# Optimization experiments

Hardware: AMD Instinct MI355X
Metric: run time of the kernel (lower is better)

## Reference

```python
import math
import jax, jax.numpy as jnp
import numpy as np

NH = 16          # num attention heads
NOPE = 128       # qk_nope_head_dim
ROPE = 64        # qk_rope_head_dim
VD = 128         # v_head_dim
QLR = 1536       # q_lora_rank
IH = 8           # index_n_heads
ID = 128         # index_head_dim
TOPK = 8         # index_topk
EPS = 1e-5


def layernorm(x, w, b):
    mu = jnp.mean(x, axis=-1, keepdims=True)
    var = jnp.mean((x - mu) ** 2, axis=-1, keepdims=True)
    return (x - mu) * jax.lax.rsqrt(var + EPS) * w + b


def rope_tables(dim, end, base=10000.0):
    freqs = 1.0 / (base ** (jnp.arange(0, dim, 2, dtype=jnp.float32) / dim))  # [dim//2]
    t = jnp.arange(end, dtype=jnp.float32)
    f = jnp.outer(t, freqs)  # [end, dim//2]
    return jnp.cos(f), jnp.sin(f)


def apply_rope(x, cos, sin):
    # x: [b, h, s, d]; cos/sin: [s, d//2] (interleaved real/imag pairs)
    xr, xi = x[..., 0::2], x[..., 1::2]
    c = cos[None, None, :, :]
    s = sin[None, None, :, :]
    or_, oi = xr * c - xi * s, xr * s + xi * c
    return jnp.stack([or_, oi], axis=-1).reshape(x.shape)


def setup_inputs() -> dict:
    key = jax.random.key(0)
    ks = jax.random.split(key, 16)
    H = 2048
    B, S = 2, 2048
    w = lambda k, shp: (jax.random.normal(k, shp, dtype=jnp.float32) * 0.02)
    return {
        "x": jax.random.normal(ks[0], (B, S, H), dtype=jnp.float32),
        "W_cq": w(ks[1], (H, QLR)),
        "q_norm_w": jnp.ones((QLR,), jnp.float32),
        "q_norm_b": jnp.zeros((QLR,), jnp.float32),
        "W_q": w(ks[2], (QLR, NH * (NOPE + ROPE))),
        "W_ckv": w(ks[3], (H, NH * (NOPE + ROPE))),
        "kv_norm_w": jnp.ones((NOPE,), jnp.float32),
        "kv_norm_b": jnp.zeros((NOPE,), jnp.float32),
        "W_kv": w(ks[4], (NOPE, NOPE + VD)),
        "W_o": w(ks[5], (NH * VD, H)),
        "W_ip": w(ks[6], (H, IH * ID)),
        "W_ig": w(ks[7], (H, IH)),
        "W_sq": w(ks[8], (ID, ID)),
        "W_sk": w(ks[9], (ID, ID)),
        "W_sv": w(ks[10], (ID, ID)),
        "W_io": w(ks[11], (ID, H)),
    }


def _forward(x, W_cq, q_norm_w, q_norm_b, W_q, W_ckv, kv_norm_w, kv_norm_b,
             W_kv, W_o, W_ip, W_ig, W_sq, W_sk, W_sv, W_io):
    B, S, H = x.shape
    # --- MLA dense path ---
    qc = layernorm(x @ W_cq, q_norm_w, q_norm_b)                  # [B,S,QLR]
    qp = (qc @ W_q).reshape(B, S, NH, NOPE + ROPE).transpose(0, 2, 1, 3)
    q_nope, q_pe = qp[..., :NOPE], qp[..., NOPE:]
    kvc = (x @ W_ckv).reshape(B, S, NH, ROPE + NOPE).transpose(0, 2, 1, 3)
    k_pe, kv_nope = kvc[..., :ROPE], kvc[..., ROPE:]
    kv_n = layernorm(kv_nope, kv_norm_w, kv_norm_b)               # [B,NH,S,NOPE]
    kvp = kv_n @ W_kv                                             # [B,NH,S,NOPE+VD]
    k_nope, v = kvp[..., :NOPE], kvp[..., NOPE:]
    cos, sin = rope_tables(ROPE, S)
    q_pe = apply_rope(q_pe, cos, sin)
    k_pe = apply_rope(k_pe, cos, sin)
    q = jnp.concatenate([q_nope, q_pe], axis=-1)                  # [B,NH,S,192]
    k = jnp.concatenate([k_nope, k_pe], axis=-1)
    scale = 1.0 / math.sqrt(NOPE + ROPE)
    scores = jnp.einsum("bhqd,bhkd->bhqk", q, k) * scale
    causal = jnp.triu(jnp.ones((S, S), dtype=bool), k=1)
    scores = jnp.where(causal[None, None], -jnp.inf, scores)
    probs = jax.nn.softmax(scores.astype(jnp.float32), axis=-1).astype(q.dtype)
    attn = jnp.einsum("bhqk,bhkd->bhqd", probs, v)                # [B,NH,S,VD]
    # --- NSA sparse path (lightning indexer) ---
    ist = (x @ W_ip).reshape(B, S, IH, ID).transpose(0, 2, 1, 3)  # [B,IH,S,ID]
    gate = (x @ W_ig).transpose(0, 2, 1)                          # [B,IH,S]
    _, top_idx = jax.lax.top_k(gate, TOPK)                        # [B,IH,TOPK]
    sel = jnp.take_along_axis(ist, top_idx[..., None], axis=2)    # [B,IH,TOPK,ID]
    sq, sk, sv = sel @ W_sq, sel @ W_sk, sel @ W_sv
    ss = jnp.einsum("bhqd,bhkd->bhqk", sq, sk) / math.sqrt(ID)    # [B,IH,TOPK,TOPK]
    sp = jax.nn.softmax(ss.astype(jnp.float32), axis=-1).astype(sq.dtype)
    so = jnp.einsum("bhqk,bhkd->bhqd", sp, sv)                    # [B,IH,TOPK,ID]
    sparse_out = so @ W_io                                        # [B,IH,TOPK,H]
    io = sparse_out.mean(axis=2)[:, :, None, :VD]                 # [B,IH,1,VD]
    io = jnp.broadcast_to(io, (B, IH, S, VD))
    io = jnp.repeat(io, NH // IH, axis=1)                         # [B,NH,S,VD]
    attn = attn + io
    out = attn.transpose(0, 2, 1, 3).reshape(B, S, NH * VD) @ W_o
    return out


def reference(x, W_cq, q_norm_w, q_norm_b, W_q, W_ckv, kv_norm_w, kv_norm_b,
              W_kv, W_o, W_ip, W_ig, W_sq, W_sk, W_sv, W_io):
    return _forward(x, W_cq, q_norm_w, q_norm_b, W_q, W_ckv, kv_norm_w,
                    kv_norm_b, W_kv, W_o, W_ip, W_ig, W_sq, W_sk, W_sv, W_io)
```

## Files before the change

### kernel.cpp

```cpp
#include <hip/hip_runtime.h>
#include <hip/hip_bf16.h>
#include <math.h>

#define NH    16
#define NOPE  128
#define ROPED 64
#define VD    128
#define QLR   1536
#define IH    8
#define ID    128
#define TOPK  8
#define EPSF  1e-5f
#define B_    2
#define S_    2048
#define H_    2048

using bf16 = __hip_bfloat16;
typedef __attribute__((ext_vector_type(8))) short short8;
typedef __attribute__((ext_vector_type(4))) short short4v;
typedef __attribute__((ext_vector_type(4))) float f32x4;

#define GLOBAL_AS __attribute__((address_space(1)))
#define LDS_AS    __attribute__((address_space(3)))

__device__ __forceinline__ float b2f(bf16 v) { return __bfloat162float(v); }
__device__ __forceinline__ bf16 f2b(float v) { return __float2bfloat16(v); }
__device__ __forceinline__ void stoC(float* p, float v) { *p = v; }
__device__ __forceinline__ void stoC(bf16* p, float v) { *p = __float2bfloat16(v); }

__global__ __launch_bounds__(256) void gate_k(const float* __restrict__ x,
                                              const float* __restrict__ Wg,
                                              float* __restrict__ gate) {
    const int t = threadIdx.x;
    const int wid = t >> 6, lane = t & 63;
    const int row = blockIdx.x * 4 + wid;
    const float* xp = x + (size_t)row * H_;

    float acc[8] = {};
    for (int k0 = 0; k0 < H_; k0 += 256) {
        const int kb = k0 + lane * 4;
        const f32x4 xv = *(const f32x4*)(xp + kb);
        const f32x4 w0 = *(const f32x4*)(Wg + (size_t)kb * 8);
        const f32x4 w1 = *(const f32x4*)(Wg + (size_t)kb * 8 + 4);
        const f32x4 w2 = *(const f32x4*)(Wg + (size_t)(kb + 1) * 8);
        const f32x4 w3 = *(const f32x4*)(Wg + (size_t)(kb + 1) * 8 + 4);
        const f32x4 w4 = *(const f32x4*)(Wg + (size_t)(kb + 2) * 8);
        const f32x4 w5 = *(const f32x4*)(Wg + (size_t)(kb + 2) * 8 + 4);
        const f32x4 w6 = *(const f32x4*)(Wg + (size_t)(kb + 3) * 8);
        const f32x4 w7 = *(const f32x4*)(Wg + (size_t)(kb + 3) * 8 + 4);
#pragma unroll
        for (int j = 0; j < 4; j++) {
            acc[j]     += xv[0] * w0[j] + xv[1] * w2[j] + xv[2] * w4[j] + xv[3] * w6[j];
            acc[4 + j] += xv[0] * w1[j] + xv[1] * w3[j] + xv[2] * w5[j] + xv[3] * w7[j];
        }
    }
#pragma unroll
    for (int j = 0; j < 8; j++) {
#pragma unroll
        for (int off = 32; off > 0; off >>= 1)
            acc[j] += __shfl_xor(acc[j], off);
    }
    if (lane == 0) {
#pragma unroll
        for (int j = 0; j < 8; j++) gate[(size_t)row * 8 + j] = acc[j];
    }
}

template <typename OT>
__global__ __launch_bounds__(256) void gemm_bt_mfma_k(const bf16* __restrict__ A,
                                                      const bf16* __restrict__ Bt,
                                                      OT* __restrict__ C,
                                                      int M, int N, int K) {
    __shared__ bf16 As[128 * 32];
    __shared__ bf16 Bs[128 * 32];
    const int t = threadIdx.x;
    const int w = t >> 6;
    const int l = t & 63;
    const int col = l & 15;
    const int quad = l >> 4;
    const int wm = w >> 1, wn = w & 1;

    const int gx = gridDim.x;
    const int nwg = gx * gridDim.y;
    const int lin = blockIdx.y * gx + blockIdx.x;
    const int work = (lin & 7) * (nwg >> 3) + (lin >> 3);
    const int row0 = (work / gx) * 128;
    const int col0 = (work % gx) * 128;

    const int rA = l >> 2;
    const int cA = (l & 3) * 8;
    const bf16* ga0 = A + (size_t)(row0 + w * 16 + rA) * K + cA;
    const bf16* ga1 = A + (size_t)(row0 + (4 + w) * 16 + rA) * K + cA;
    const bf16* gb0 = Bt + (size_t)(col0 + w * 16 + rA) * K + cA;
    const bf16* gb1 = Bt + (size_t)(col0 + (4 + w) * 16 + rA) * K + cA;
    bf16* lA0 = &As[w * 512];
    bf16* lA1 = &As[(4 + w) * 512];
    bf16* lB0 = &Bs[w * 512];
    bf16* lB1 = &Bs[(4 + w) * 512];

    f32x4 acc[4][4];
#pragma unroll
    for (int i = 0; i < 4; i++)
#pragma unroll
        for (int j = 0; j < 4; j++) acc[i][j] = (f32x4){0.f, 0.f, 0.f, 0.f};

    for (int k0 = 0; k0 < K; k0 += 32) {
        __syncthreads();
        __builtin_amdgcn_global_load_lds((const GLOBAL_AS void*)(ga0 + k0),
                                         (LDS_AS void*)lA0, 16, 0, 0);
        __builtin_amdgcn_global_load_lds((const GLOBAL_AS void*)(ga1 + k0),
                                         (LDS_AS void*)lA1, 16, 0, 0);
        __builtin_amdgcn_global_load_lds((const GLOBAL_AS void*)(gb0 + k0),
                                         (LDS_AS void*)lB0, 16, 0, 0);
        __builtin_amdgcn_global_load_lds((const GLOBAL_AS void*)(gb1 + k0),
                                         (LDS_AS void*)lB1, 16, 0, 0);
        __syncthreads();

        short8 af[4], bfr[4];
#pragma unroll
        for (int i = 0; i < 4; i++) {
            af[i]  = *(const short8*)&As[(wm * 64 + i * 16 + col) * 32 + quad * 8];
            bfr[i] = *(const short8*)&Bs[(wn * 64 + i * 16 + col) * 32 + quad * 8];
        }
#pragma unroll
        for (int i = 0; i < 4; i++)
#pragma unroll
            for (int j = 0; j < 4; j++)
                acc[i][j] = __builtin_amdgcn_mfma_f32_16x16x32_bf16(af[i], bfr[j], acc[i][j], 0, 0, 0);
    }

#pragma unroll
    for (int i = 0; i < 4; i++)
#pragma unroll
        for (int j = 0; j < 4; j++)
#pragma unroll
            for (int r = 0; r < 4; r++) {
                const int gr = row0 + wm * 64 + i * 16 + quad * 4 + r;
                const int gc = col0 + wn * 64 + j * 16 + col;
                stoC(C + (size_t)gr * N + gc, acc[i][j][r]);
            }
}

__global__ __launch_bounds__(256) void gemm_kv_k(const bf16* __restrict__ A,
                                                 const bf16* __restrict__ Bt,
                                                 bf16* __restrict__ kvc,
                                                 bf16* __restrict__ VbT) {
    __shared__ bf16 As[128 * 32];
    __shared__ bf16 Bs[128 * 32];
    const int K = 128;
    const int t = threadIdx.x;
    const int w = t >> 6;
    const int l = t & 63;
    const int col = l & 15;
    const int quad = l >> 4;
    const int wm = w >> 1, wn = w & 1;

    const int gx = gridDim.x;
    const int nwg = gx * gridDim.y;
    const int lin = blockIdx.y * gx + blockIdx.x;
    const int work = (lin & 7) * (nwg >> 3) + (lin >> 3);
    const int row0 = (work / gx) * 128;
    const int col0 = (work % gx) * 128;

    const int rA = l >> 2;
    const int cA = (l & 3) * 8;
    const bf16* ga0 = A + (size_t)(row0 + w * 16 + rA) * K + cA;
    const bf16* ga1 = A + (size_t)(row0 + (4 + w) * 16 + rA) * K + cA;
    const bf16* gb0 = Bt + (size_t)(col0 + w * 16 + rA) * K + cA;
    const bf16* gb1 = Bt + (size_t)(col0 + (4 + w) * 16 + rA) * K + cA;
    bf16* lA0 = &As[w * 512];
    bf16* lA1 = &As[(4 + w) * 512];
    bf16* lB0 = &Bs[w * 512];
    bf16* lB1 = &Bs[(4 + w) * 512];

    f32x4 acc[4][4];
#pragma unroll
    for (int i = 0; i < 4; i++)
#pragma unroll
        for (int j = 0; j < 4; j++) acc[i][j] = (f32x4){0.f, 0.f, 0.f, 0.f};

    for (int k0 = 0; k0 < K; k0 += 32) {
        __syncthreads();
        __builtin_amdgcn_global_load_lds((const GLOBAL_AS void*)(ga0 + k0),
                                         (LDS_AS void*)lA0, 16, 0, 0);
        __builtin_amdgcn_global_load_lds((const GLOBAL_AS void*)(ga1 + k0),
                                         (LDS_AS void*)lA1, 16, 0, 0);
        __builtin_amdgcn_global_load_lds((const GLOBAL_AS void*)(gb0 + k0),
                                         (LDS_AS void*)lB0, 16, 0, 0);
        __builtin_amdgcn_global_load_lds((const GLOBAL_AS void*)(gb1 + k0),
                                         (LDS_AS void*)lB1, 16, 0, 0);
        __syncthreads();

        short8 af[4], bfr[4];
#pragma unroll
        for (int i = 0; i < 4; i++) {
            af[i]  = *(const short8*)&As[(wm * 64 + i * 16 + col) * 32 + quad * 8];
            bfr[i] = *(const short8*)&Bs[(wn * 64 + i * 16 + col) * 32 + quad * 8];
        }
#pragma unroll
        for (int i = 0; i < 4; i++)
#pragma unroll
            for (int j = 0; j < 4; j++)
                acc[i][j] = __builtin_amdgcn_mfma_f32_16x16x32_bf16(af[i], bfr[j], acc[i][j], 0, 0, 0);
    }

    if (col0 == 0) {
#pragma unroll
        for (int i = 0; i < 4; i++)
#pragma unroll
            for (int j = 0; j < 4; j++)
#pragma unroll
                for (int r = 0; r < 4; r++) {
                    const int gr = row0 + wm * 64 + i * 16 + quad * 4 + r;
                    const int gc = wn * 64 + j * 16 + col;
                    kvc[(size_t)gr * 192 + gc] = f2b(acc[i][j][r]);
                }
    } else {
        const int bb = row0 >> 15;
        const int ssb = ((row0 >> 4) & (S_ - 1)) + wm * 4;
#pragma unroll
        for (int j = 0; j < 4; j++) {
            const int dv = wn * 64 + j * 16 + col;
#pragma unroll
            for (int r = 0; r < 4; r++) {
                const int hh = quad * 4 + r;
                short4v pk;
#pragma unroll
                for (int i = 0; i < 4; i++) {
                    bf16 v = f2b(acc[i][j][r]);
                    pk[i] = *(short*)&v;
                }
                *(short4v*)&VbT[((size_t)(bb * NH + hh) * 128 + dv) * S_ + ssb] = pk;
            }
        }
    }
}

__global__ __launch_bounds__(256) void kv_ln_k(bf16* __restrict__ kvc,
                                               const float* __restrict__ knw,
                                               const float* __restrict__ knb,
                                               bf16* __restrict__ kvn) {
    const int idx = blockIdx.x * 4 + (threadIdx.x >> 6);
    const int lane = threadIdx.x & 63;
    const int s = (idx >> 4) & (S_ - 1);
    const size_t base = (size_t)idx * 192;

    const float v0 = b2f(kvc[base + 64 + lane]);
    const float v1 = b2f(kvc[base + 128 + lane]);
    float xr = 0.f, xi = 0.f;
    if (lane < 32) { xr = b2f(kvc[base + 2 * lane]); xi = b2f(kvc[base + 2 * lane + 1]); }

    float s1 = v0 + v1, s2 = v0 * v0 + v1 * v1;
#pragma unroll
    for (int off = 32; off > 0; off >>= 1) {
        s1 += __shfl_xor(s1, off);
        s2 += __shfl_xor(s2, off);
    }
    const float mu = s1 * (1.f / 128.f);
    const float rinv = rsqrtf(s2 * (1.f / 128.f) - mu * mu + EPSF);
    kvn[(size_t)idx * 128 + lane]      = f2b((v0 - mu) * rinv * knw[lane] + knb[lane]);
    kvn[(size_t)idx * 128 + lane + 64] = f2b((v1 - mu) * rinv * knw[lane + 64] + knb[lane + 64]);

    if (lane < 32) {
        const float freq = exp2f(-0.41524101186092014f * (float)lane);
        const float ang = (float)s * freq;
        float sn, c; sincosf(ang, &sn, &c);
        kvc[base + 128 + 2 * lane]     = f2b(xr * c - xi * sn);
        kvc[base + 128 + 2 * lane + 1] = f2b(xr * sn + xi * c);
    }
}

__global__ __launch_bounds__(256) void cast_bf16_k(const float* __restrict__ X,
                                                   bf16* __restrict__ Y, int n4) {
    for (int i = blockIdx.x * 256 + threadIdx.x; i < n4; i += gridDim.x * 256) {
        const f32x4 v = ((const f32x4*)X)[i];
        short4v o;
#pragma unroll
        for (int j = 0; j < 4; j++) {
            bf16 b = f2b(v[j]);
            o[j] = *(short*)&b;
        }
        ((short4v*)Y)[i] = o;
    }
}

__global__ __launch_bounds__(256) void transpose_cast_k(const float* __restrict__ W,
                                                        bf16* __restrict__ Wt,
                                                        int K, int N) {
    __shared__ float tile[32][33];
    const int t = threadIdx.x;
    const int tx = t & 31, ty = t >> 5;
    const int n0 = blockIdx.x * 32;
    const int k0 = blockIdx.y * 32;
#pragma unroll
    for (int i = 0; i < 4; i++)
        tile[ty + 8 * i][tx] = W[(size_t)(k0 + ty + 8 * i) * N + n0 + tx];
    __syncthreads();
#pragma unroll
    for (int i = 0; i < 4; i++)
        Wt[(size_t)(n0 + ty + 8 * i) * K + k0 + tx] = f2b(tile[tx][ty + 8 * i]);
}

__global__ __launch_bounds__(256) void layernorm_cast_k(const float* __restrict__ X,
                                                        const float* __restrict__ w,
                                                        const float* __restrict__ b,
                                                        bf16* __restrict__ Y,
                                                        int L) {
    __shared__ float r1[256], r2[256];
    const int row = blockIdx.x;
    const int t = threadIdx.x;
    const float* xp = X + (size_t)row * L;
    bf16* yp = Y + (size_t)row * L;
    float s1 = 0.f, s2 = 0.f;
    for (int j = t; j < L; j += 256) { const float v = xp[j]; s1 += v; s2 += v * v; }
    r1[t] = s1; r2[t] = s2; __syncthreads();
    for (int off = 128; off > 0; off >>= 1) {
        if (t < off) { r1[t] += r1[t + off]; r2[t] += r2[t + off]; }
        __syncthreads();
    }
    const float mu   = r1[0] / (float)L;
    const float var  = r2[0] / (float)L - mu * mu;
    const float rinv = rsqrtf(var + EPSF);
    for (int j = t; j < L; j += 256)
        yp[j] = f2b((xp[j] - mu) * rinv * w[j] + b[j]);
}

__global__ __launch_bounds__(256) void q_rope_k(bf16* __restrict__ qp) {
    const int total = B_ * S_ * NH * 32;
    for (int p = blockIdx.x * 256 + threadIdx.x; p < total; p += gridDim.x * 256) {
        const int j = p & 31;
        const int row = p >> 5;
        const int sr = row >> 4;
        const int s = sr & (S_ - 1);
        const size_t base = (size_t)row * 192 + 128 + 2 * j;
        const float xr = b2f(qp[base]);
        const float xi = b2f(qp[base + 1]);
        const float freq = exp2f(-0.41524101186092014f * (float)j);
        const float ang = (float)s * freq;
        float sn, c; sincosf(ang, &sn, &c);
        qp[base]     = f2b(xr * c - xi * sn);
        qp[base + 1] = f2b(xr * sn + xi * c);
    }
}

__global__ __launch_bounds__(256) void sparse_k(const float* __restrict__ gate,
                                                const float* __restrict__ ist,
                                                const float* __restrict__ Wsq,
                                                const float* __restrict__ Wsk,
                                                const float* __restrict__ Wsv,
                                                const float* __restrict__ Wio,
                                                float* __restrict__ io) {
    __shared__ float g[S_];
    __shared__ float sel[TOPK][ID];
    __shared__ float sq[TOPK][ID], sk[TOPK][ID], sv[TOPK][ID];
    __shared__ float sp[TOPK][TOPK];
    __shared__ float ms[ID];
    __shared__ float rv[256];
    __shared__ int ri[256];
    __shared__ int sidx[TOPK];
    const int bi = blockIdx.x;
    const int ih = bi % IH;
    const int b = bi / IH;
    const int t = threadIdx.x;

    for (int s = t; s < S_; s += 256) g[s] = gate[(size_t)(b * S_ + s) * IH + ih];
    __syncthreads();

    for (int r = 0; r < TOPK; r++) {
        float bv = -INFINITY; int bx = S_;
        for (int s = t; s < S_; s += 256) {
            const float v = g[s];
            if (v > bv) { bv = v; bx = s; }
        }
        rv[t] = bv; ri[t] = bx; __syncthreads();
        for (int off = 128; off > 0; off >>= 1) {
            if (t < off) {
                const float v2 = rv[t + off]; const int i2 = ri[t + off];
                if (v2 > rv[t] || (v2 == rv[t] && i2 < ri[t])) { rv[t] = v2; ri[t] = i2; }
            }
            __syncthreads();
        }
        if (t == 0) { sidx[r] = ri[0]; g[ri[0]] = -INFINITY; }
        __syncthreads();
    }

    for (int i = t; i < TOPK * ID; i += 256) {
        const int r = i >> 7, d = i & 127;
        sel[r][d] = ist[((size_t)(b * S_ + sidx[r]) * IH + ih) * ID + d];
    }
    __syncthreads();

    for (int i = t; i < TOPK * ID; i += 256) {
        const int r = i >> 7, n = i & 127;
        float aq = 0.f, ak = 0.f, av = 0.f;
        for (int k = 0; k < 128; k++) {
            const float s = sel[r][k];
            aq += s * Wsq[k * ID + n];
            ak += s * Wsk[k * ID + n];
            av += s * Wsv[k * ID + n];
        }
        sq[r][n] = aq; sk[r][n] = ak; sv[r][n] = av;
    }
    __syncthreads();

    if (t < TOPK * TOPK) {
        const int r = t >> 3, c = t & 7;
        float a = 0.f;
        for (int k = 0; k < 128; k++) a += sq[r][k] * sk[c][k];
        sp[r][c] = a * 0.08838834764831845f;
    }
    __syncthreads();

    if (t < TOPK) {
        float m = -INFINITY;
        for (int c = 0; c < 8; c++) m = fmaxf(m, sp[t][c]);
        float e[8]; float sum = 0.f;
        for (int c = 0; c < 8; c++) { e[c] = expf(sp[t][c] - m); sum += e[c]; }
        for (int c = 0; c < 8; c++) sp[t][c] = e[c] / sum;
    }
    __syncthreads();

    if (t < ID) {
        float acc = 0.f;
        for (int r = 0; r < 8; r++) {
            float so = 0.f;
            for (int c = 0; c < 8; c++) so += sp[r][c] * sv[c][t];
            acc += so;
        }
        ms[t] = acc * 0.125f;
    }
    __syncthreads();

    if (t < ID) {
        float acc = 0.f;
        for (int k = 0; k < 128; k++) acc += ms[k] * Wio[(size_t)k * H_ + t];
        io[((size_t)b * IH + ih) * ID + t] = acc;
    }
}

__global__ __launch_bounds__(256) void attn_mfma_k(const bf16* __restrict__ Qp,
                                                   const bf16* __restrict__ Kc,
                                                   const bf16* __restrict__ VbT,
                                                   const float* __restrict__ io,
                                                   bf16* __restrict__ O) {
    __shared__ unsigned short Kt[64 * 200];
    __shared__ unsigned short Vt[128 * 72];
    __shared__ unsigned short Ps[4 * 16 * 72];
    __shared__ float io_s[128];

    const int lin = blockIdx.x + 16 * blockIdx.y + 256 * blockIdx.z;
    const int swz = (lin & 7) * 64 + (lin >> 3);
    const int pairi = swz & 15;
    const int h = (swz >> 4) & 15;
    const int b = swz >> 8;

    const int t = threadIdx.x;
    const int lane = t & 63;
    const int wq = t >> 6;
    const int col = lane & 15;
    const int quad = lane >> 4;

    if (t < 128) io_s[t] = io[((size_t)b * IH + (h >> 1)) * ID + t];

    const float scale = 0.07216878364870322f;
    const bf16* vplane = VbT + (size_t)(b * NH + h) * 128 * (size_t)S_;

#pragma unroll 1
    for (int ti = 0; ti < 2; ti++) {
        const int qt = (ti == 0) ? pairi : 31 - pairi;
        const int q0 = qt * 64;

        short8 qfrag[6];
        {
            const int q = q0 + wq * 16 + col;
            const short8* qrow = (const short8*)(Qp + ((size_t)(b * S_ + q) * NH + h) * 192);
#pragma unroll
            for (int kc = 0; kc < 6; kc++) qfrag[kc] = qrow[kc * 4 + quad];
        }

        float m_r[4], l_r[4];
#pragma unroll
        for (int r = 0; r < 4; r++) { m_r[r] = -1e30f; l_r[r] = 0.f; }
        f32x4 accO[8];
#pragma unroll
        for (int nt = 0; nt < 8; nt++) accO[nt] = (f32x4){0.f, 0.f, 0.f, 0.f};

        const int nkt = qt + 1;

        for (int kt = 0; kt < nkt; kt++) {
            const int kt0 = kt * 64;
            __syncthreads();
            {
                const int kr = t >> 2;
                const int c0 = (t & 3) * 48;
                const short8* src = (const short8*)(Kc + ((size_t)(b * S_ + kt0 + kr) * NH + h) * 192 + c0);
                short8* dst = (short8*)&Kt[kr * 200 + c0];
#pragma unroll
                for (int c = 0; c < 6; c++) dst[c] = src[c];
            }
            {
                const int ki0 = (t & 7) * 8;
#pragma unroll
                for (int p = 0; p < 4; p++) {
                    const int dv = p * 32 + (t >> 3);
                    const short8 vv = *(const short8*)(vplane + (size_t)dv * S_ + kt0 + ki0);
                    *(short8*)&Vt[dv * 72 + ki0] = vv;
                }
            }
            __syncthreads();

            f32x4 s[4];
            __builtin_amdgcn_s_setprio(1);
#pragma unroll
            for (int nt = 0; nt < 4; nt++) {
                f32x4 acc = (f32x4){0.f, 0.f, 0.f, 0.f};
#pragma unroll
                for (int kc = 0; kc < 6; kc++) {
                    const short8 kf = *(const short8*)&Kt[(nt * 16 + col) * 200 + kc * 32 + quad * 8];
                    acc = __builtin_amdgcn_mfma_f32_16x16x32_bf16(qfrag[kc], kf, acc, 0, 0, 0);
                }
                s[nt] = acc;
            }
            __builtin_amdgcn_s_setprio(0);
#pragma unroll
            for (int nt = 0; nt < 4; nt++)
#pragma unroll
                for (int r = 0; r < 4; r++) {
                    const int kg = kt0 + nt * 16 + col;
                    const int qg = q0 + wq * 16 + quad * 4 + r;
                    const float v = s[nt][r] * scale;
                    s[nt][r] = (kg > qg) ? -1e30f : v;
                }
            float alpha[4];
#pragma unroll
            for (int r = 0; r < 4; r++) {
                float mt = fmaxf(fmaxf(s[0][r], s[1][r]), fmaxf(s[2][r], s[3][r]));
                mt = fmaxf(mt, __shfl_xor(mt, 1));
                mt = fmaxf(mt, __shfl_xor(mt, 2));
                mt = fmaxf(mt, __shfl_xor(mt, 4));
                mt = fmaxf(mt, __shfl_xor(mt, 8));
                const float mn = fmaxf(m_r[r], mt);
                alpha[r] = __expf(m_r[r] - mn);
                m_r[r] = mn;
                float rs = 0.f;
#pragma unroll
                for (int nt = 0; nt < 4; nt++) {
                    const float p = __expf(s[nt][r] - mn);
                    s[nt][r] = p;
                    rs += p;
                }
                rs += __shfl_xor(rs, 1);
                rs += __shfl_xor(rs, 2);
                rs += __shfl_xor(rs, 4);
                rs += __shfl_xor(rs, 8);
                l_r[r] = l_r[r] * alpha[r] + rs;
            }
            {
                unsigned short* pw = &Ps[wq * 1152];
#pragma unroll
                for (int nt = 0; nt < 4; nt++)
#pragma unroll
                    for (int r = 0; r < 4; r++) {
                        bf16 hv = f2b(s[nt][r]);
                        pw[(quad * 4 + r) * 72 + nt * 16 + col] = *(unsigned short*)&hv;
                    }
            }
            short8 pf[2];
#pragma unroll
            for (int kk = 0; kk < 2; kk++)
                pf[kk] = *(const short8*)&Ps[wq * 1152 + col * 72 + kk * 32 + quad * 8];
#pragma unroll
            for (int nt = 0; nt < 8; nt++)
#pragma unroll
                for (int r = 0; r < 4; r++) accO[nt][r] *= alpha[r];
            __builtin_amdgcn_s_setprio(1);
#pragma unroll
            for (int nt = 0; nt < 8; nt++) {
#pragma unroll
                for (int kk = 0; kk < 2; kk++) {
                    const short8 vf = *(const short8*)&Vt[(nt * 16 + col) * 72 + kk * 32 + quad * 8];
                    accO[nt] = __builtin_amdgcn_mfma_f32_16x16x32_bf16(pf[kk], vf, accO[nt], 0, 0, 0);
                }
            }
            __builtin_amdgcn_s_setprio(0);
        }

        float rinv[4];
#pragma unroll
        for (int r = 0; r < 4; r++) rinv[r] = 1.f / l_r[r];
#pragma unroll
        for (int nt = 0; nt < 8; nt++) {
            const int dv = nt * 16 + col;
            const float iov = io_s[dv];
#pragma unroll
            for (int r = 0; r < 4; r++) {
                const int q = q0 + wq * 16 + quad * 4 + r;
                O[((size_t)(b * S_ + q) * NH + h) * VD + dv] = f2b(accO[nt][r] * rinv[r] + iov);
            }
        }
    }
}

extern "C" void kernel_launch(void* const* d_in, const int* in_sizes, int n_in,
                              void* d_out, int out_size, void* d_ws, size_t ws_size,
                              hipStream_t stream) {
    const float* x      = (const float*)d_in[0];
    const float* W_cq   = (const float*)d_in[1];
    const float* qn_w   = (const float*)d_in[2];
    const float* qn_b   = (const float*)d_in[3];
    const float* W_q    = (const float*)d_in[4];
    const float* W_ckv  = (const float*)d_in[5];
    const float* kvn_w  = (const float*)d_in[6];
    const float* kvn_b  = (const float*)d_in[7];
    const float* W_kv   = (const float*)d_in[8];
    const float* W_o    = (const float*)d_in[9];
    const float* W_ip   = (const float*)d_in[10];
    const float* W_ig   = (const float*)d_in[11];
    const float* W_sq   = (const float*)d_in[12];
    const float* W_sk   = (const float*)d_in[13];
    const float* W_sv   = (const float*)d_in[14];
    const float* W_io   = (const float*)d_in[15];
    float* out = (float*)d_out;

    const int M = B_ * S_;

    char* wsb = (char*)d_ws;
    float* rbig  = (float*)wsb;
    bf16*  kvn   = (bf16*)(wsb + 16777216);
    bf16*  qp    = (bf16*)(wsb + 33554432);
    bf16*  kvc   = (bf16*)(wsb + 58720256);
    bf16*  cqb   = (bf16*)(wsb + 58720256);
    bf16*  VbT   = (bf16*)(wsb + 83886080);
    bf16*  Wt    = (bf16*)(wsb + 83886080);
    float* gate  = (float*)(wsb + 100663296);
    bf16*  WkvT  = (bf16*)(wsb + 100663296);
    float* iob   = (float*)(wsb + 100794368);
    float* cq    = rbig;
    float* ist   = rbig;
    bf16*  attnb = (bf16*)rbig;
    bf16*  xb    = (bf16*)d_out;

    dim3 blk(256);

    cast_bf16_k<<<dim3(2048), blk, 0, stream>>>(x, xb, M * H_ / 4);

    transpose_cast_k<<<dim3(QLR / 32, H_ / 32), blk, 0, stream>>>(W_cq, Wt, H_, QLR);
    gemm_bt_mfma_k<float><<<dim3(QLR / 128, M / 128), blk, 0, stream>>>(xb, Wt, cq, M, QLR, H_);
    layernorm_cast_k<<<dim3(M), blk, 0, stream>>>(cq, qn_w, qn_b, cqb, QLR);

    transpose_cast_k<<<dim3(3072 / 32, QLR / 32), blk, 0, stream>>>(W_q, Wt, QLR, 3072);
    gemm_bt_mfma_k<bf16><<<dim3(3072 / 128, M / 128), blk, 0, stream>>>(cqb, Wt, qp, M, 3072, QLR);

    transpose_cast_k<<<dim3(3072 / 32, H_ / 32), blk, 0, stream>>>(W_ckv, Wt, H_, 3072);
    gemm_bt_mfma_k<bf16><<<dim3(3072 / 128, M / 128), blk, 0, stream>>>(xb, Wt, kvc, M, 3072, H_);

    transpose_cast_k<<<dim3(1024 / 32, H_ / 32), blk, 0, stream>>>(W_ip, Wt, H_, 1024);
    gemm_bt_mfma_k<float><<<dim3(1024 / 128, M / 128), blk, 0, stream>>>(xb, Wt, ist, M, IH * ID, H_);

    gate_k<<<dim3(M / 4), blk, 0, stream>>>(x, W_ig, gate);

    q_rope_k<<<dim3(2048), blk, 0, stream>>>(qp);

    kv_ln_k<<<dim3(B_ * S_ * NH / 4), blk, 0, stream>>>(kvc, kvn_w, kvn_b, kvn);

    sparse_k<<<dim3(B_ * IH), blk, 0, stream>>>(gate, ist, W_sq, W_sk, W_sv, W_io, iob);

    transpose_cast_k<<<dim3(256 / 32, 128 / 32), blk, 0, stream>>>(W_kv, WkvT, 128, 256);
    gemm_kv_k<<<dim3(2, (B_ * S_ * NH) / 128), blk, 0, stream>>>(kvn, WkvT, kvc, VbT);

    attn_mfma_k<<<dim3(16, NH, B_), blk, 0, stream>>>(qp, kvc, VbT, iob, attnb);

    transpose_cast_k<<<dim3(H_ / 32, H_ / 32), blk, 0, stream>>>(W_o, Wt, H_, H_);
    gemm_bt_mfma_k<float><<<dim3(H_ / 128, M / 128), blk, 0, stream>>>(attnb, Wt, out, M, H_, H_);
}
```

Baseline: 685.1 us.

## Register-prefetch next K/V tile and skip rescaling with lazy softmax max

The attention kernel now loads the next K and V tile into registers while the current tile's MFMAs run, so global-load latency overlaps compute instead of stalling before each tile. The running-max update is made lazy: the max and the accumulator rescale only change when the new tile max exceeds the old one by more than a threshold. The launch bounds also request 3 blocks per CU, and the io values are read straight from global memory. The extra prefetch registers compete with the occupancy hint, which may cause spills, and the lazy max lets exponentials grow up to e^8 before rescaling.

```diff
diff --git a/kernel.cpp b/kernel.cpp
--- a/kernel.cpp
+++ b/kernel.cpp
@@ -438,15 +438,14 @@
     }
 }
 
-__global__ __launch_bounds__(256) void attn_mfma_k(const bf16* __restrict__ Qp,
-                                                   const bf16* __restrict__ Kc,
-                                                   const bf16* __restrict__ VbT,
-                                                   const float* __restrict__ io,
-                                                   bf16* __restrict__ O) {
+__global__ __launch_bounds__(256, 3) void attn_mfma_k(const bf16* __restrict__ Qp,
+                                                      const bf16* __restrict__ Kc,
+                                                      const bf16* __restrict__ VbT,
+                                                      const float* __restrict__ io,
+                                                      bf16* __restrict__ O) {
     __shared__ unsigned short Kt[64 * 200];
     __shared__ unsigned short Vt[128 * 72];
     __shared__ unsigned short Ps[4 * 16 * 72];
-    __shared__ float io_s[128];
 
     const int lin = blockIdx.x + 16 * blockIdx.y + 256 * blockIdx.z;
     const int swz = (lin & 7) * 64 + (lin >> 3);
@@ -460,10 +459,13 @@
     const int col = lane & 15;
     const int quad = lane >> 4;
 
-    if (t < 128) io_s[t] = io[((size_t)b * IH + (h >> 1)) * ID + t];
-
     const float scale = 0.07216878364870322f;
     const bf16* vplane = VbT + (size_t)(b * NH + h) * 128 * (size_t)S_;
+
+    const int kr = t >> 2;
+    const int kc0 = (t & 3) * 48;
+    const int vki0 = (t & 7) * 8;
+    const int vdv = t >> 3;
 
 #pragma unroll 1
     for (int ti = 0; ti < 2; ti++) {
@@ -487,27 +489,38 @@
 
         const int nkt = qt + 1;
 
+        short8 kreg[6], vreg[4];
+        {
+            const short8* ksrc = (const short8*)(Kc + ((size_t)(b * S_ + kr) * NH + h) * 192 + kc0);
+#pragma unroll
+            for (int c = 0; c < 6; c++) kreg[c] = ksrc[c];
+#pragma unroll
+            for (int p = 0; p < 4; p++)
+                vreg[p] = *(const short8*)(vplane + (size_t)(p * 32 + vdv) * S_ + vki0);
+        }
+
         for (int kt = 0; kt < nkt; kt++) {
             const int kt0 = kt * 64;
             __syncthreads();
             {
-                const int kr = t >> 2;
-                const int c0 = (t & 3) * 48;
-                const short8* src = (const short8*)(Kc + ((size_t)(b * S_ + kt0 + kr) * NH + h) * 192 + c0);
-                short8* dst = (short8*)&Kt[kr * 200 + c0];
-#pragma unroll
-                for (int c = 0; c < 6; c++) dst[c] = src[c];
-            }
-            {
-                const int ki0 = (t & 7) * 8;
-#pragma unroll
-                for (int p = 0; p < 4; p++) {
-                    const int dv = p * 32 + (t >> 3);
-                    const short8 vv = *(const short8*)(vplane + (size_t)dv * S_ + kt0 + ki0);
-                    *(short8*)&Vt[dv * 72 + ki0] = vv;
-                }
+                short8* dst = (short8*)&Kt[kr * 200 + kc0];
+#pragma unroll
+                for (int c = 0; c < 6; c++) dst[c] = kreg[c];
+#pragma unroll
+                for (int p = 0; p < 4; p++)
+                    *(short8*)&Vt[(p * 32 + vdv) * 72 + vki0] = vreg[p];
             }
             __syncthreads();
+
+            if (kt + 1 < nkt) {
+                const int nk0 = kt0 + 64;
+                const short8* ksrc = (const short8*)(Kc + ((size_t)(b * S_ + nk0 + kr) * NH + h) * 192 + kc0);
+#pragma unroll
+                for (int c = 0; c < 6; c++) kreg[c] = ksrc[c];
+#pragma unroll
+                for (int p = 0; p < 4; p++)
+                    vreg[p] = *(const short8*)(vplane + (size_t)(p * 32 + vdv) * S_ + nk0 + vki0);
+            }
 
             f32x4 s[4];
             __builtin_amdgcn_s_setprio(1);
@@ -539,8 +552,9 @@
                 mt = fmaxf(mt, __shfl_xor(mt, 2));
                 mt = fmaxf(mt, __shfl_xor(mt, 4));
                 mt = fmaxf(mt, __shfl_xor(mt, 8));
-                const float mn = fmaxf(m_r[r], mt);
-                alpha[r] = __expf(m_r[r] - mn);
+                const bool need = (mt > m_r[r] + 8.f);
+                const float mn = need ? mt : m_r[r];
+                alpha[r] = need ? __expf(m_r[r] - mn) : 1.f;
                 m_r[r] = mn;
                 float rs = 0.f;
 #pragma unroll
@@ -569,10 +583,12 @@
 #pragma unroll
             for (int kk = 0; kk < 2; kk++)
                 pf[kk] = *(const short8*)&Ps[wq * 1152 + col * 72 + kk * 32 + quad * 8];
-#pragma unroll
-            for (int nt = 0; nt < 8; nt++)
-#pragma unroll
-                for (int r = 0; r < 4; r++) accO[nt][r] *= alpha[r];
+            if (!(alpha[0] == 1.f && alpha[1] == 1.f && alpha[2] == 1.f && alpha[3] == 1.f)) {
+#pragma unroll
+                for (int nt = 0; nt < 8; nt++)
+#pragma unroll
+                    for (int r = 0; r < 4; r++) accO[nt][r] *= alpha[r];
+            }
             __builtin_amdgcn_s_setprio(1);
 #pragma unroll
             for (int nt = 0; nt < 8; nt++) {
@@ -585,13 +601,14 @@
             __builtin_amdgcn_s_setprio(0);
         }
 
+        const float* iorow = io + ((size_t)b * IH + (h >> 1)) * ID;
         float rinv[4];
 #pragma unroll
         for (int r = 0; r < 4; r++) rinv[r] = 1.f / l_r[r];
 #pragma unroll
         for (int nt = 0; nt < 8; nt++) {
             const int dv = nt * 16 + col;
-            const float iov = io_s[dv];
+            const float iov = iorow[dv];
 #pragma unroll
             for (int r = 0; r < 4; r++) {
                 const int q = q0 + wq * 16 + quad * 4 + r;
```

Result: slower. 711.2 us (+3.8%).
